# Optimization experiments

Hardware: AMD Instinct MI355X
Metric: run time of the kernel (lower is better)

Reference implementation:

```python
import jax, jax.numpy as jnp
import numpy as np
from jax import lax

DN = ('NCHW', 'OIHW', 'NCHW')


def _dwconv(x, w, pad_h, pad_w):
    # depthwise conv: feature_group_count == channels
    C = x.shape[1]
    return lax.conv_general_dilated(
        x, w, window_strides=(1, 1),
        padding=[(pad_h, pad_h), (pad_w, pad_w)],
        dimension_numbers=DN, feature_group_count=C)


def setup_inputs() -> dict:
    key = jax.random.key(0)
    ks = jax.random.split(key, 6)
    B, C, H, W = 8, 64, 256, 256
    K = 21
    x = jax.random.normal(ks[0], (B, C, H, W), dtype=jnp.float32)
    local_w = jax.random.normal(ks[1], (C, 1, 5, 5), dtype=jnp.float32) * (2.0 / 25) ** 0.5
    h_w = jax.random.normal(ks[2], (C, 1, 1, K), dtype=jnp.float32) * (2.0 / K) ** 0.5
    v_w = jax.random.normal(ks[3], (C, 1, K, 1), dtype=jnp.float32) * (2.0 / K) ** 0.5
    pw_w = jax.random.normal(ks[4], (C, C, 1, 1), dtype=jnp.float32) * (1.0 / C) ** 0.5
    gamma = jnp.ones((C,), dtype=jnp.float32)
    beta = jnp.zeros((C,), dtype=jnp.float32)
    mean = jnp.zeros((C,), dtype=jnp.float32)
    var = jnp.ones((C,), dtype=jnp.float32)
    return {"x": x, "local_w": local_w, "h_w": h_w, "v_w": v_w,
            "pw_w": pw_w, "gamma": gamma, "beta": beta, "mean": mean, "var": var}


def reference(x, local_w, h_w, v_w, pw_w, gamma, beta, mean, var):
    eps = 1e-5
    attn = _dwconv(x, local_w, 2, 2)        # 5x5 depthwise
    attn = _dwconv(attn, h_w, 0, 10)        # 1x21 depthwise
    attn = _dwconv(attn, v_w, 10, 0)        # 21x1 depthwise
    attn = lax.conv_general_dilated(        # 1x1 pointwise (full mix)
        attn, pw_w, (1, 1), [(0, 0), (0, 0)], dimension_numbers=DN)
    # BatchNorm (inference mode with running stats) fused with sigmoid gate
    inv = gamma * lax.rsqrt(var + eps)
    attn = attn * inv[None, :, None, None] + (beta - mean * inv)[None, :, None, None]
    return x * jax.nn.sigmoid(attn)
```

## Files before the change

### kernel.cpp

```cpp
#include <hip/hip_runtime.h>
#include <hip/hip_bf16.h>

#define BB 8
#define CC 64
#define HH 256
#define WW 256

__device__ __forceinline__ unsigned short f2bf(float f) {
    __hip_bfloat16 h = __float2bfloat16(f);
    return *reinterpret_cast<unsigned short*>(&h);
}
__device__ __forceinline__ float bf2f(unsigned short u) {
    unsigned int v = ((unsigned int)u) << 16;
    float r;
    __builtin_memcpy(&r, &v, 4);
    return r;
}
__device__ __forceinline__ float bflo(unsigned int u) {
    unsigned int v = u << 16;
    float r; __builtin_memcpy(&r, &v, 4); return r;
}
__device__ __forceinline__ float bfhi(unsigned int u) {
    unsigned int v = u & 0xffff0000u;
    float r; __builtin_memcpy(&r, &v, 4); return r;
}

__global__ __launch_bounds__(512) void k1_local_h(
        const float* __restrict__ x, const float* __restrict__ lw,
        const float* __restrict__ hw, unsigned short* __restrict__ a2out) {
    const int strip = blockIdx.x;
    const int bc    = blockIdx.y;
    const int c     = bc & (CC - 1);
    const int y0    = strip * 8;
    const int tid   = threadIdx.x;

    __shared__ float4 xs4[12][66];
    __shared__ float4 a1_4[8][70];

    const float* xbase = x + (size_t)bc * (HH * WW);

    if (tid < 48) {
        int rr = tid / 6, g = tid % 6;
        a1_4[rr][g < 3 ? g : 64 + g] = make_float4(0.f, 0.f, 0.f, 0.f);
    }

    for (int i = tid; i < 12 * 66; i += 512) {
        int rr = i / 66, g = i - rr * 66;
        int gy = y0 - 2 + rr;
        float4 v = make_float4(0.f, 0.f, 0.f, 0.f);
        if (gy >= 0 && gy < HH && g >= 1 && g <= 64)
            v = *reinterpret_cast<const float4*>(xbase + (size_t)gy * WW + 4 * (g - 1));
        xs4[rr][g] = v;
    }
    __syncthreads();

    const int r = tid >> 6;
    const int l = tid & 63;
    const float* lwc = lw + c * 25;

    float acc[4] = {0.f, 0.f, 0.f, 0.f};
    #pragma unroll
    for (int ky = 0; ky < 5; ++ky) {
        float4 g0 = xs4[r + ky][l];
        float4 g1 = xs4[r + ky][l + 1];
        float4 g2 = xs4[r + ky][l + 2];
        float rowv[12] = {g0.x, g0.y, g0.z, g0.w, g1.x, g1.y, g1.z, g1.w,
                          g2.x, g2.y, g2.z, g2.w};
        #pragma unroll
        for (int kx = 0; kx < 5; ++kx) {
            float wv = lwc[ky * 5 + kx];
            #pragma unroll
            for (int j = 0; j < 4; ++j)
                acc[j] = fmaf(wv, rowv[j + kx + 2], acc[j]);
        }
    }
    a1_4[r][l + 3] = make_float4(acc[0], acc[1], acc[2], acc[3]);
    __syncthreads();

    float w28[28];
    #pragma unroll
    for (int t = 0; t < 7; ++t) {
        float4 g = a1_4[r][l + t];
        w28[4 * t + 0] = g.x; w28[4 * t + 1] = g.y;
        w28[4 * t + 2] = g.z; w28[4 * t + 3] = g.w;
    }
    float o[4] = {0.f, 0.f, 0.f, 0.f};
    const float* hwc = hw + c * 21;
    #pragma unroll
    for (int k = 0; k < 21; ++k) {
        float wv = hwc[k];
        #pragma unroll
        for (int j = 0; j < 4; ++j)
            o[j] = fmaf(wv, w28[j + k + 2], o[j]);
    }

    unsigned short* dst = a2out + (size_t)(bc * HH + y0 + r) * WW + 4 * l;
    ushort4 pk;
    pk.x = f2bf(o[0]); pk.y = f2bf(o[1]); pk.z = f2bf(o[2]); pk.w = f2bf(o[3]);
    *reinterpret_cast<ushort4*>(dst) = pk;
}

__global__ __launch_bounds__(256) void k2a_v(
        const unsigned short* __restrict__ a2, const float* __restrict__ vw,
        unsigned short* __restrict__ a3) {
    const int strip = blockIdx.x;
    const int bc    = blockIdx.y;
    const int c     = bc & (CC - 1);
    const int y0    = strip * 64;
    const int tid   = threadIdx.x;

    __shared__ unsigned short lds[84][256];

    const unsigned short* sbase = a2 + (size_t)bc * (HH * WW);
    for (int i = tid; i < 84 * 32; i += 256) {
        int row = i >> 5, g = i & 31;
        int gy = y0 - 10 + row;
        uint4 v = make_uint4(0u, 0u, 0u, 0u);
        if (gy >= 0 && gy < HH)
            v = *reinterpret_cast<const uint4*>(sbase + (size_t)gy * WW + g * 8);
        *reinterpret_cast<uint4*>(&lds[row][g * 8]) = v;
    }
    __syncthreads();

    const float* vwc = vw + c * 21;
    float w[21];
    #pragma unroll
    for (int k = 0; k < 21; ++k) w[k] = vwc[k];

    const int cg = tid & 31;
    const int rg = tid >> 5;
    unsigned short* dst = a3 + (size_t)bc * (HH * WW)
                        + (size_t)(y0 + rg * 8) * WW + cg * 8;

    #pragma unroll 1
    for (int i = 0; i < 8; ++i) {
        float s0 = 0.f, s1 = 0.f, s2 = 0.f, s3 = 0.f;
        float s4 = 0.f, s5 = 0.f, s6 = 0.f, s7 = 0.f;
        #pragma unroll
        for (int k = 0; k < 21; ++k) {
            uint4 u = *reinterpret_cast<const uint4*>(&lds[rg * 8 + i + k][cg * 8]);
            float wk = w[k];
            s0 = fmaf(wk, bflo(u.x), s0); s1 = fmaf(wk, bfhi(u.x), s1);
            s2 = fmaf(wk, bflo(u.y), s2); s3 = fmaf(wk, bfhi(u.y), s3);
            s4 = fmaf(wk, bflo(u.z), s4); s5 = fmaf(wk, bfhi(u.z), s5);
            s6 = fmaf(wk, bflo(u.w), s6); s7 = fmaf(wk, bfhi(u.w), s7);
        }
        uint4 o;
        o.x = (unsigned int)f2bf(s0) | ((unsigned int)f2bf(s1) << 16);
        o.y = (unsigned int)f2bf(s2) | ((unsigned int)f2bf(s3) << 16);
        o.z = (unsigned int)f2bf(s4) | ((unsigned int)f2bf(s5) << 16);
        o.w = (unsigned int)f2bf(s6) | ((unsigned int)f2bf(s7) << 16);
        *reinterpret_cast<uint4*>(dst + (size_t)i * WW) = o;
    }
}

__global__ __launch_bounds__(256) void k2b_pw(
        const unsigned short* __restrict__ a3, const float* __restrict__ x,
        const float* __restrict__ pw, const float* __restrict__ gamma,
        const float* __restrict__ beta, const float* __restrict__ mean,
        const float* __restrict__ var, float* __restrict__ out) {
    const int y   = blockIdx.x;
    const int b   = blockIdx.y;
    const int tid = threadIdx.x;

    __shared__ unsigned short a3s[64][256];

    const unsigned short* abase = a3 + ((size_t)b * CC * HH + y) * WW;
    for (int i = tid; i < 64 * 64; i += 256) {
        int ci = i >> 6, q = (i & 63) << 2;
        ushort4 v = *reinterpret_cast<const ushort4*>(abase + (size_t)ci * HH * WW + q);
        *reinterpret_cast<ushort4*>(&a3s[ci][q]) = v;
    }
    __syncthreads();

    const int wu = __builtin_amdgcn_readfirstlane(tid >> 6);
    const int l  = tid & 63;

    float acc[64];
    #pragma unroll
    for (int i = 0; i < 64; ++i) acc[i] = 0.f;

    #pragma unroll 4
    for (int ci = 0; ci < 64; ++ci) {
        ushort4 raw = *reinterpret_cast<const ushort4*>(&a3s[ci][l << 2]);
        float p0 = bf2f(raw.x), p1 = bf2f(raw.y), p2 = bf2f(raw.z), p3 = bf2f(raw.w);
        #pragma unroll
        for (int j = 0; j < 16; ++j) {
            float wv = pw[(wu * 16 + j) * 64 + ci];
            acc[j * 4 + 0] = fmaf(wv, p0, acc[j * 4 + 0]);
            acc[j * 4 + 1] = fmaf(wv, p1, acc[j * 4 + 1]);
            acc[j * 4 + 2] = fmaf(wv, p2, acc[j * 4 + 2]);
            acc[j * 4 + 3] = fmaf(wv, p3, acc[j * 4 + 3]);
        }
    }

    #pragma unroll
    for (int j = 0; j < 16; ++j) {
        int co = wu * 16 + j;
        float inv = gamma[co] * rsqrtf(var[co] + 1e-5f);
        float sh  = beta[co] - mean[co] * inv;
        size_t off = (((size_t)b * CC + co) * HH + y) * WW + (l << 2);
        float4 xv = *reinterpret_cast<const float4*>(x + off);
        float4 r;
        float a;
        a = acc[j * 4 + 0] * inv + sh; r.x = xv.x / (1.f + __expf(-a));
        a = acc[j * 4 + 1] * inv + sh; r.y = xv.y / (1.f + __expf(-a));
        a = acc[j * 4 + 2] * inv + sh; r.z = xv.z / (1.f + __expf(-a));
        a = acc[j * 4 + 3] * inv + sh; r.w = xv.w / (1.f + __expf(-a));
        *reinterpret_cast<float4*>(out + off) = r;
    }
}

extern "C" void kernel_launch(void* const* d_in, const int* in_sizes, int n_in,
                              void* d_out, int out_size, void* d_ws, size_t ws_size,
                              hipStream_t stream) {
    const float* x     = (const float*)d_in[0];
    const float* lw    = (const float*)d_in[1];
    const float* hw    = (const float*)d_in[2];
    const float* vw    = (const float*)d_in[3];
    const float* pw    = (const float*)d_in[4];
    const float* gamma = (const float*)d_in[5];
    const float* beta  = (const float*)d_in[6];
    const float* mean  = (const float*)d_in[7];
    const float* var   = (const float*)d_in[8];
    float* out = (float*)d_out;

    unsigned short* ws1 = (unsigned short*)d_ws;
    unsigned short* ws2 = ws1 + (size_t)BB * CC * HH * WW;

    k1_local_h<<<dim3(HH / 8, BB * CC), 512, 0, stream>>>(x, lw, hw, ws1);
    k2a_v<<<dim3(HH / 64, BB * CC), 256, 0, stream>>>(ws1, vw, ws2);
    k2b_pw<<<dim3(HH, BB), 256, 0, stream>>>(ws2, x, pw, gamma, beta, mean, var, out);
}
```

Measured before the change: 420.8 us.

## Enlarge k1 row strips with register blocking, split k2a columns, vectorize pw weights

k1 now handles 32-row strips instead of 8, which cuts the fraction of halo rows loaded. Each thread computes 2 rows by 8 columns, so each loaded x row feeds two output rows through the 5x5 filter, and the 1x21 pass emits 8 outputs per thread. k2a splits every 64-row strip into two 128-column halves, doubling the block count and halving LDS per block. k2b_pw processes four input channels per step with float4 weight loads to reduce scalar load overhead. The costs are higher register pressure in k1 and larger shared memory per block (about 74KB), which may lower occupancy.

After: 445.0 us. 5.8% more time.

```diff
diff --git a/kernel.cpp b/kernel.cpp
--- a/kernel.cpp
+++ b/kernel.cpp
@@ -31,20 +31,19 @@
     const int strip = blockIdx.x;
     const int bc    = blockIdx.y;
     const int c     = bc & (CC - 1);
-    const int y0    = strip * 8;
+    const int y0    = strip * 32;
     const int tid   = threadIdx.x;
 
-    __shared__ float4 xs4[12][66];
-    __shared__ float4 a1_4[8][70];
+    __shared__ float4 xs4[36][66];
+    __shared__ float4 a1_4[32][70];
 
     const float* xbase = x + (size_t)bc * (HH * WW);
 
-    if (tid < 48) {
+    if (tid < 192) {
         int rr = tid / 6, g = tid % 6;
         a1_4[rr][g < 3 ? g : 64 + g] = make_float4(0.f, 0.f, 0.f, 0.f);
     }
-
-    for (int i = tid; i < 12 * 66; i += 512) {
+    for (int i = tid; i < 36 * 66; i += 512) {
         int rr = i / 66, g = i - rr * 66;
         int gy = y0 - 2 + rr;
         float4 v = make_float4(0.f, 0.f, 0.f, 0.f);
@@ -54,66 +53,93 @@
     }
     __syncthreads();
 
-    const int r = tid >> 6;
-    const int l = tid & 63;
+    const int cg = tid & 31;
+    const int rp = tid >> 5;
     const float* lwc = lw + c * 25;
 
-    float acc[4] = {0.f, 0.f, 0.f, 0.f};
-    #pragma unroll
-    for (int ky = 0; ky < 5; ++ky) {
-        float4 g0 = xs4[r + ky][l];
-        float4 g1 = xs4[r + ky][l + 1];
-        float4 g2 = xs4[r + ky][l + 2];
-        float rowv[12] = {g0.x, g0.y, g0.z, g0.w, g1.x, g1.y, g1.z, g1.w,
-                          g2.x, g2.y, g2.z, g2.w};
-        #pragma unroll
-        for (int kx = 0; kx < 5; ++kx) {
-            float wv = lwc[ky * 5 + kx];
+    float acc0[8], acc1[8];
+    #pragma unroll
+    for (int j = 0; j < 8; ++j) { acc0[j] = 0.f; acc1[j] = 0.f; }
+
+    #pragma unroll
+    for (int t = 0; t < 6; ++t) {
+        float4 g0 = xs4[2 * rp + t][2 * cg + 0];
+        float4 g1 = xs4[2 * rp + t][2 * cg + 1];
+        float4 g2 = xs4[2 * rp + t][2 * cg + 2];
+        float4 g3 = xs4[2 * rp + t][2 * cg + 3];
+        float f[16] = {g0.x, g0.y, g0.z, g0.w, g1.x, g1.y, g1.z, g1.w,
+                       g2.x, g2.y, g2.z, g2.w, g3.x, g3.y, g3.z, g3.w};
+        if (t < 5) {
             #pragma unroll
-            for (int j = 0; j < 4; ++j)
-                acc[j] = fmaf(wv, rowv[j + kx + 2], acc[j]);
-        }
-    }
-    a1_4[r][l + 3] = make_float4(acc[0], acc[1], acc[2], acc[3]);
-    __syncthreads();
-
-    float w28[28];
-    #pragma unroll
-    for (int t = 0; t < 7; ++t) {
-        float4 g = a1_4[r][l + t];
-        w28[4 * t + 0] = g.x; w28[4 * t + 1] = g.y;
-        w28[4 * t + 2] = g.z; w28[4 * t + 3] = g.w;
-    }
-    float o[4] = {0.f, 0.f, 0.f, 0.f};
+            for (int kx = 0; kx < 5; ++kx) {
+                float wv = lwc[t * 5 + kx];
+                #pragma unroll
+                for (int j = 0; j < 8; ++j)
+                    acc0[j] = fmaf(wv, f[j + kx + 2], acc0[j]);
+            }
+        }
+        if (t >= 1) {
+            #pragma unroll
+            for (int kx = 0; kx < 5; ++kx) {
+                float wv = lwc[(t - 1) * 5 + kx];
+                #pragma unroll
+                for (int j = 0; j < 8; ++j)
+                    acc1[j] = fmaf(wv, f[j + kx + 2], acc1[j]);
+            }
+        }
+    }
+    a1_4[2 * rp + 0][2 * cg + 3] = make_float4(acc0[0], acc0[1], acc0[2], acc0[3]);
+    a1_4[2 * rp + 0][2 * cg + 4] = make_float4(acc0[4], acc0[5], acc0[6], acc0[7]);
+    a1_4[2 * rp + 1][2 * cg + 3] = make_float4(acc1[0], acc1[1], acc1[2], acc1[3]);
+    a1_4[2 * rp + 1][2 * cg + 4] = make_float4(acc1[4], acc1[5], acc1[6], acc1[7]);
+    __syncthreads();
+
     const float* hwc = hw + c * 21;
     #pragma unroll
-    for (int k = 0; k < 21; ++k) {
-        float wv = hwc[k];
-        #pragma unroll
-        for (int j = 0; j < 4; ++j)
-            o[j] = fmaf(wv, w28[j + k + 2], o[j]);
-    }
-
-    unsigned short* dst = a2out + (size_t)(bc * HH + y0 + r) * WW + 4 * l;
-    ushort4 pk;
-    pk.x = f2bf(o[0]); pk.y = f2bf(o[1]); pk.z = f2bf(o[2]); pk.w = f2bf(o[3]);
-    *reinterpret_cast<ushort4*>(dst) = pk;
+    for (int row = 0; row < 2; ++row) {
+        float fw[32];
+        #pragma unroll
+        for (int t2 = 0; t2 < 8; ++t2) {
+            float4 g = a1_4[2 * rp + row][2 * cg + t2];
+            fw[4 * t2 + 0] = g.x; fw[4 * t2 + 1] = g.y;
+            fw[4 * t2 + 2] = g.z; fw[4 * t2 + 3] = g.w;
+        }
+        float o[8];
+        #pragma unroll
+        for (int j = 0; j < 8; ++j) o[j] = 0.f;
+        #pragma unroll
+        for (int k = 0; k < 21; ++k) {
+            float wv = hwc[k];
+            #pragma unroll
+            for (int j = 0; j < 8; ++j)
+                o[j] = fmaf(wv, fw[j + k + 2], o[j]);
+        }
+        unsigned short* dst = a2out + (size_t)(bc * HH + y0 + 2 * rp + row) * WW + 8 * cg;
+        uint4 pk;
+        pk.x = (unsigned)f2bf(o[0]) | ((unsigned)f2bf(o[1]) << 16);
+        pk.y = (unsigned)f2bf(o[2]) | ((unsigned)f2bf(o[3]) << 16);
+        pk.z = (unsigned)f2bf(o[4]) | ((unsigned)f2bf(o[5]) << 16);
+        pk.w = (unsigned)f2bf(o[6]) | ((unsigned)f2bf(o[7]) << 16);
+        *reinterpret_cast<uint4*>(dst) = pk;
+    }
 }
 
 __global__ __launch_bounds__(256) void k2a_v(
         const unsigned short* __restrict__ a2, const float* __restrict__ vw,
         unsigned short* __restrict__ a3) {
-    const int strip = blockIdx.x;
+    const int bx    = blockIdx.x;
+    const int strip = bx >> 1;
+    const int x0    = (bx & 1) * 128;
     const int bc    = blockIdx.y;
     const int c     = bc & (CC - 1);
     const int y0    = strip * 64;
     const int tid   = threadIdx.x;
 
-    __shared__ unsigned short lds[84][256];
-
-    const unsigned short* sbase = a2 + (size_t)bc * (HH * WW);
-    for (int i = tid; i < 84 * 32; i += 256) {
-        int row = i >> 5, g = i & 31;
+    __shared__ unsigned short lds[84][128];
+
+    const unsigned short* sbase = a2 + (size_t)bc * (HH * WW) + x0;
+    for (int i = tid; i < 84 * 16; i += 256) {
+        int row = i >> 4, g = i & 15;
         int gy = y0 - 10 + row;
         uint4 v = make_uint4(0u, 0u, 0u, 0u);
         if (gy >= 0 && gy < HH)
@@ -127,18 +153,18 @@
     #pragma unroll
     for (int k = 0; k < 21; ++k) w[k] = vwc[k];
 
-    const int cg = tid & 31;
-    const int rg = tid >> 5;
+    const int cg = tid & 15;
+    const int rg = tid >> 4;
     unsigned short* dst = a3 + (size_t)bc * (HH * WW)
-                        + (size_t)(y0 + rg * 8) * WW + cg * 8;
+                        + (size_t)(y0 + rg * 4) * WW + x0 + cg * 8;
 
     #pragma unroll 1
-    for (int i = 0; i < 8; ++i) {
+    for (int i = 0; i < 4; ++i) {
         float s0 = 0.f, s1 = 0.f, s2 = 0.f, s3 = 0.f;
         float s4 = 0.f, s5 = 0.f, s6 = 0.f, s7 = 0.f;
         #pragma unroll
         for (int k = 0; k < 21; ++k) {
-            uint4 u = *reinterpret_cast<const uint4*>(&lds[rg * 8 + i + k][cg * 8]);
+            uint4 u = *reinterpret_cast<const uint4*>(&lds[rg * 4 + i + k][cg * 8]);
             float wk = w[k];
             s0 = fmaf(wk, bflo(u.x), s0); s1 = fmaf(wk, bfhi(u.x), s1);
             s2 = fmaf(wk, bflo(u.y), s2); s3 = fmaf(wk, bfhi(u.y), s3);
@@ -180,17 +206,37 @@
     #pragma unroll
     for (int i = 0; i < 64; ++i) acc[i] = 0.f;
 
-    #pragma unroll 4
-    for (int ci = 0; ci < 64; ++ci) {
-        ushort4 raw = *reinterpret_cast<const ushort4*>(&a3s[ci][l << 2]);
-        float p0 = bf2f(raw.x), p1 = bf2f(raw.y), p2 = bf2f(raw.z), p3 = bf2f(raw.w);
+    const float* wbase = pw + (size_t)(wu * 16) * 64;
+
+    #pragma unroll
+    for (int ch = 0; ch < 16; ++ch) {
+        ushort4 q0 = *reinterpret_cast<const ushort4*>(&a3s[4 * ch + 0][l << 2]);
+        ushort4 q1 = *reinterpret_cast<const ushort4*>(&a3s[4 * ch + 1][l << 2]);
+        ushort4 q2 = *reinterpret_cast<const ushort4*>(&a3s[4 * ch + 2][l << 2]);
+        ushort4 q3 = *reinterpret_cast<const ushort4*>(&a3s[4 * ch + 3][l << 2]);
+        float p0x = bf2f(q0.x), p0y = bf2f(q0.y), p0z = bf2f(q0.z), p0w = bf2f(q0.w);
+        float p1x = bf2f(q1.x), p1y = bf2f(q1.y), p1z = bf2f(q1.z), p1w = bf2f(q1.w);
+        float p2x = bf2f(q2.x), p2y = bf2f(q2.y), p2z = bf2f(q2.z), p2w = bf2f(q2.w);
+        float p3x = bf2f(q3.x), p3y = bf2f(q3.y), p3z = bf2f(q3.z), p3w = bf2f(q3.w);
         #pragma unroll
         for (int j = 0; j < 16; ++j) {
-            float wv = pw[(wu * 16 + j) * 64 + ci];
-            acc[j * 4 + 0] = fmaf(wv, p0, acc[j * 4 + 0]);
-            acc[j * 4 + 1] = fmaf(wv, p1, acc[j * 4 + 1]);
-            acc[j * 4 + 2] = fmaf(wv, p2, acc[j * 4 + 2]);
-            acc[j * 4 + 3] = fmaf(wv, p3, acc[j * 4 + 3]);
+            float4 w4 = *reinterpret_cast<const float4*>(wbase + (size_t)j * 64 + 4 * ch);
+            acc[j * 4 + 0] = fmaf(w4.x, p0x, acc[j * 4 + 0]);
+            acc[j * 4 + 0] = fmaf(w4.y, p1x, acc[j * 4 + 0]);
+            acc[j * 4 + 0] = fmaf(w4.z, p2x, acc[j * 4 + 0]);
+            acc[j * 4 + 0] = fmaf(w4.w, p3x, acc[j * 4 + 0]);
+            acc[j * 4 + 1] = fmaf(w4.x, p0y, acc[j * 4 + 1]);
+            acc[j * 4 + 1] = fmaf(w4.y, p1y, acc[j * 4 + 1]);
+            acc[j * 4 + 1] = fmaf(w4.z, p2y, acc[j * 4 + 1]);
+            acc[j * 4 + 1] = fmaf(w4.w, p3y, acc[j * 4 + 1]);
+            acc[j * 4 + 2] = fmaf(w4.x, p0z, acc[j * 4 + 2]);
+            acc[j * 4 + 2] = fmaf(w4.y, p1z, acc[j * 4 + 2]);
+            acc[j * 4 + 2] = fmaf(w4.z, p2z, acc[j * 4 + 2]);
+            acc[j * 4 + 2] = fmaf(w4.w, p3z, acc[j * 4 + 2]);
+            acc[j * 4 + 3] = fmaf(w4.x, p0w, acc[j * 4 + 3]);
+            acc[j * 4 + 3] = fmaf(w4.y, p1w, acc[j * 4 + 3]);
+            acc[j * 4 + 3] = fmaf(w4.z, p2w, acc[j * 4 + 3]);
+            acc[j * 4 + 3] = fmaf(w4.w, p3w, acc[j * 4 + 3]);
         }
     }
 
@@ -228,7 +274,7 @@
     unsigned short* ws1 = (unsigned short*)d_ws;
     unsigned short* ws2 = ws1 + (size_t)BB * CC * HH * WW;
 
-    k1_local_h<<<dim3(HH / 8, BB * CC), 512, 0, stream>>>(x, lw, hw, ws1);
-    k2a_v<<<dim3(HH / 64, BB * CC), 256, 0, stream>>>(ws1, vw, ws2);
+    k1_local_h<<<dim3(HH / 32, BB * CC), 512, 0, stream>>>(x, lw, hw, ws1);
+    k2a_v<<<dim3(8, BB * CC), 256, 0, stream>>>(ws1, vw, ws2);
     k2b_pw<<<dim3(HH, BB), 256, 0, stream>>>(ws2, x, pw, gamma, beta, mean, var, out);
 }
```
